# Kernel tuning notes

Measured on AMD Instinct MI355X. Metric: run time of the kernel, lower is better.

## Reference

```python
import jax, jax.numpy as jnp
import numpy as np

N = 100000   # nodes per graph (50k users + 50k items)
E = 1600000  # edges per graph
D = 128      # feature / hidden dim
B = 100000   # train pairs per domain
NUM_USER = 50000
LAMBDA = 1.0


def setup_inputs() -> dict:
    key = jax.random.key(0)
    ks = jax.random.split(key, 24)
    s = 1.0 / np.sqrt(D)
    return {
        "feats_s": jax.random.normal(ks[0], (N, D), jnp.float32),
        "feats_t": jax.random.normal(ks[1], (N, D), jnp.float32),
        "W1": jax.random.normal(ks[2], (D, D), jnp.float32) * s,
        "b1": jnp.zeros((D,), jnp.float32),
        "W2": jax.random.normal(ks[3], (D, D), jnp.float32) * s,
        "b2": jnp.zeros((D,), jnp.float32),
        "cls_W": jax.random.normal(ks[4], (2 * D, 1), jnp.float32) * s,
        "cls_b": jnp.zeros((1,), jnp.float32),
        "du_W": jax.random.normal(ks[5], (D, 1), jnp.float32) * s,
        "du_b": jnp.zeros((1,), jnp.float32),
        "di_W": jax.random.normal(ks[6], (D, 1), jnp.float32) * s,
        "di_b": jnp.zeros((1,), jnp.float32),
        "edge_src_s": jax.random.randint(ks[7], (E,), 0, N, jnp.int32),
        "edge_dst_s": jax.random.randint(ks[8], (E,), 0, N, jnp.int32),
        "edge_src_t": jax.random.randint(ks[9], (E,), 0, N, jnp.int32),
        "edge_dst_t": jax.random.randint(ks[10], (E,), 0, N, jnp.int32),
        "user_s": jax.random.randint(ks[11], (B,), 0, NUM_USER, jnp.int32),
        "item_s": jax.random.randint(ks[12], (B,), 0, NUM_USER, jnp.int32),
        "labels_s": jax.random.randint(ks[13], (B,), 0, 2, jnp.int32),
        "user_t": jax.random.randint(ks[14], (B,), 0, NUM_USER, jnp.int32),
        "item_t": jax.random.randint(ks[15], (B,), 0, NUM_USER, jnp.int32),
        "labels_t": jax.random.randint(ks[16], (B,), 0, 2, jnp.int32),
        "num_user_ds": NUM_USER,
        "num_user_dt": NUM_USER,
    }


def _gcn_layer(x, W, b, src, dst, dinv):
    # PyG GCNConv: out[i] = sum_{j->i} dinv[j]*dinv[i] * (x @ W)[j] + b
    h = x @ W
    norm = (dinv[src] * dinv[dst])[:, None]
    return jax.ops.segment_sum(h[src] * norm, dst, num_segments=x.shape[0]) + b


def _encode(x, src, dst, W1, b1, W2, b2):
    n = x.shape[0]
    sl = jnp.arange(n, dtype=src.dtype)            # self loops
    src = jnp.concatenate([src, sl])
    dst = jnp.concatenate([dst, sl])
    deg = jax.ops.segment_sum(jnp.ones_like(dst, dtype=x.dtype), dst, num_segments=n)
    dinv = jax.lax.rsqrt(jnp.maximum(deg, 1.0))    # deg >= 1 due to self loops
    h = jax.nn.relu(_gcn_layer(x, W1, b1, src, dst, dinv))
    return _gcn_layer(h, W2, b2, src, dst, dinv)   # dropout is identity at eval


def _bce_from_logits(z, y):
    # mean BCE on sigmoid(z), numerically stable
    return jnp.mean(y * jax.nn.softplus(-z) + (1.0 - y) * jax.nn.softplus(z))


def reference(feats_s, feats_t, W1, b1, W2, b2, cls_W, cls_b, du_W, du_b, di_W, di_b,
              edge_src_s, edge_dst_s, edge_src_t, edge_dst_t,
              user_s, item_s, labels_s, user_t, item_t, labels_t,
              num_user_ds, num_user_dt):
    x_ds = _encode(feats_s, edge_src_s, edge_dst_s, W1, b1, W2, b2)
    x_dt = _encode(feats_t, edge_src_t, edge_dst_t, W1, b1, W2, b2)

    ufs = x_ds[user_s]
    ifs = x_ds[item_s + num_user_ds]
    uft = x_dt[user_t]
    ift = x_dt[item_t + num_user_dt]

    z_s = (jnp.concatenate([ufs, ifs], axis=1) @ cls_W).reshape(-1) + cls_b[0]
    z_t = (jnp.concatenate([uft, ift], axis=1) @ cls_W).reshape(-1) + cls_b[0]
    clf_loss = _bce_from_logits(z_s, labels_s.astype(jnp.float32)) + \
               _bce_from_logits(z_t, labels_t.astype(jnp.float32))

    cu_s = jax.nn.sigmoid((ufs @ du_W).reshape(-1) + du_b[0])
    cu_t = jax.nn.sigmoid((uft @ du_W).reshape(-1) + du_b[0])
    ci_s = jax.nn.sigmoid((ifs @ di_W).reshape(-1) + di_b[0])
    ci_t = jax.nn.sigmoid((ift @ di_W).reshape(-1) + di_b[0])
    domain_loss = jnp.abs(jnp.mean(cu_s) - jnp.mean(cu_t)) + \
                  jnp.abs(jnp.mean(ci_s) - jnp.mean(ci_t))

    return clf_loss + LAMBDA * domain_loss
```

## Files before the change

kernel.cpp:

```cpp
#include <hip/hip_runtime.h>

#define D 128
#define NB 512
#define BSLACK 4112
#define CHUNK 8

typedef __attribute__((ext_vector_type(8))) short bf16x8;
typedef __attribute__((ext_vector_type(4))) float f32x4;
typedef __attribute__((ext_vector_type(2))) float f32x2;
typedef __attribute__((ext_vector_type(4))) int i32x4;

static __device__ inline unsigned pack_bf16x2(float a, float b) {
    unsigned ua = __float_as_uint(a);
    unsigned ub = __float_as_uint(b);
    ua += 0x7fffu + ((ua >> 16) & 1u);
    ub += 0x7fffu + ((ub >> 16) & 1u);
    return (ua >> 16) | (ub & 0xffff0000u);
}

__global__ __launch_bounds__(256) void bh_k(const int* __restrict__ dst_s,
                                            const int* __restrict__ dst_t,
                                            int* __restrict__ bcnt, int E) {
    int d = blockIdx.y;
    const int* dst = d ? dst_t : dst_s;
    __shared__ int h[NB];
    for (int i = threadIdx.x; i < NB; i += 256) h[i] = 0;
    __syncthreads();
    int stride = gridDim.x * 256;
    for (int e = blockIdx.x * 256 + threadIdx.x; e < E; e += stride)
        atomicAdd(&h[dst[e] >> 8], 1);
    __syncthreads();
    for (int i = threadIdx.x; i < NB; i += 256)
        if (h[i]) atomicAdd(&bcnt[d * NB + i], h[i]);
}

__global__ __launch_bounds__(1024) void scanB_k(const int* __restrict__ bcnt,
                                                int* __restrict__ bbase,
                                                int* __restrict__ cursor) {
    __shared__ int sh[1024];
    int t = threadIdx.x;
    int v = bcnt[t];
    sh[t] = v;
    __syncthreads();
    for (int o = 1; o < 1024; o <<= 1) {
        int x = (t >= o) ? sh[t - o] : 0;
        __syncthreads();
        sh[t] += x;
        __syncthreads();
    }
    int ex = sh[t] - v;
    bbase[t] = ex; cursor[t] = ex;
    if (t == 1023) bbase[1024] = sh[1023];
}

__global__ __launch_bounds__(256) void bin_k(const int* __restrict__ src_s,
                                             const int* __restrict__ dst_s,
                                             const int* __restrict__ src_t,
                                             const int* __restrict__ dst_t,
                                             int* __restrict__ cursor,
                                             unsigned* __restrict__ pairs, int E) {
    int d = blockIdx.y;
    const int* src = d ? src_t : src_s;
    const int* dst = d ? dst_t : dst_s;
    int* cur = cursor + d * NB;
    __shared__ int h[NB];
    __shared__ int gb[NB];
    int t0 = blockIdx.x * 2048;
    if (t0 >= E) return;
    for (int i = threadIdx.x; i < NB; i += 256) h[i] = 0;
    __syncthreads();
    int rank[8]; unsigned pk[8]; short bk[8];
    #pragma unroll
    for (int j = 0; j < 8; ++j) {
        int e = t0 + j * 256 + threadIdx.x;
        if (e < E) {
            int dd = dst[e], s = src[e];
            bk[j] = (short)(dd >> 8);
            pk[j] = (unsigned)s | ((unsigned)(dd & 255) << 24);
            rank[j] = atomicAdd(&h[dd >> 8], 1);
        } else bk[j] = -1;
    }
    __syncthreads();
    for (int i = threadIdx.x; i < NB; i += 256)
        gb[i] = h[i] ? atomicAdd(&cur[i], h[i]) : 0;
    __syncthreads();
    #pragma unroll
    for (int j = 0; j < 8; ++j)
        if (bk[j] >= 0) pairs[gb[bk[j]] + rank[j]] = pk[j];
}

__global__ __launch_bounds__(256) void csrb_k(const unsigned* __restrict__ pairs,
                                              const int* __restrict__ bbase,
                                              int2* __restrict__ nspan,
                                              float* __restrict__ dinv,
                                              int* __restrict__ csr, int N) {
    int d = blockIdx.y, bx = blockIdx.x, t = threadIdx.x;
    int g = d * NB + bx;
    int e0 = bbase[g], e1 = bbase[g + 1];
    int cbase = ((e0 + 15) & ~15) + g * BSLACK;
    float* dv = dinv + (size_t)d * (N + 1);
    int2* ns = nspan + (size_t)d * N;
    __shared__ int lh[256];
    __shared__ int lex[256];
    __shared__ int lc[256];
    lh[t] = 0; lc[t] = 0;
    __syncthreads();
    for (int e = e0 + t; e < e1; e += 256)
        atomicAdd(&lh[pairs[e] >> 24], 1);
    __syncthreads();
    int node = (bx << 8) + t;
    bool valid = node < N;
    int deg = lh[t];
    int pdeg = valid ? (((deg + 16) >> 4) << 4) : 0;
    lex[t] = pdeg;
    __syncthreads();
    for (int o = 1; o < 256; o <<= 1) {
        int x = (t >= o) ? lex[t - o] : 0;
        __syncthreads();
        lex[t] += x;
        __syncthreads();
    }
    int start = cbase + lex[t] - pdeg;
    if (valid) {
        ns[node] = make_int2(start, start + pdeg);
        dv[node] = rsqrtf((float)(deg + 1));
    }
    lex[t] = start;
    __syncthreads();
    for (int e = e0 + t; e < e1; e += 256) {
        unsigned p = pairs[e];
        int dn = p >> 24;
        int rank = atomicAdd(&lc[dn], 1);
        csr[lex[dn] + rank] = (int)(p & 0xffffffu);
    }
    __syncthreads();
    if (valid) {
        int b = lex[t];
        csr[b + deg] = node;
        for (int k = deg + 1; k < pdeg; ++k) csr[b + k] = N;
    }
    if (bx == 0 && t == 0) dv[N] = 0.f;
}

__global__ __launch_bounds__(256) void packW_k(const float* __restrict__ W1,
                                               const float* __restrict__ W2,
                                               unsigned short* __restrict__ wp1,
                                               unsigned short* __restrict__ wp2) {
    const float* W = blockIdx.x ? W2 : W1;
    unsigned short* wp = blockIdx.x ? wp2 : wp1;
    for (int idx = threadIdx.x; idx < 2048; idx += 256) {
        int f = idx >> 6, lane = idx & 63;
        int t = f >> 2, c = f & 3;
        int q = lane >> 4, nn = lane & 15;
        #pragma unroll
        for (int j = 0; j < 8; ++j) {
            unsigned u = __float_as_uint(W[(c * 32 + q * 8 + j) * 128 + t * 16 + nn]);
            u += 0x7fffu + ((u >> 16) & 1u);
            wp[idx * 8 + j] = (unsigned short)(u >> 16);
        }
    }
}

__global__ __launch_bounds__(256) void gemm_mfma(const void* __restrict__ xs,
                                                 const void* __restrict__ xt,
                                                 const unsigned short* __restrict__ wp,
                                                 unsigned* __restrict__ hb,
                                                 const float* __restrict__ dinv,
                                                 int N, int in_bf16) {
    int d = blockIdx.y;
    const void* xin = d ? xt : xs;
    unsigned* out = hb + (size_t)d * (N + 1) * 32;
    const float* dv = dinv + (size_t)d * (N + 1);
    __shared__ float cs[64 * 132];
    int tid = threadIdx.x;
    int wave = tid >> 6, lane = tid & 63;
    int quad = lane >> 4, nn = lane & 15;
    long long blockbase = (long long)blockIdx.x * 64;
    long long ar = blockbase + wave * 16 + nn;
    if (ar > N - 1) ar = N - 1;

    bf16x8 a[4];
    if (in_bf16) {
        const uint4* xr = (const uint4*)((const unsigned short*)xin + ar * 128);
        #pragma unroll
        for (int c = 0; c < 4; ++c) {
            union { uint4 u; bf16x8 v; } cv;
            cv.u = xr[c * 4 + quad];
            a[c] = cv.v;
        }
    } else {
        const float4* xr = (const float4*)((const float*)xin + ar * 128);
        #pragma unroll
        for (int c = 0; c < 4; ++c) {
            float4 lo = xr[c * 8 + quad * 2];
            float4 hi = xr[c * 8 + quad * 2 + 1];
            union { bf16x8 v; unsigned u[4]; } au;
            au.u[0] = pack_bf16x2(lo.x, lo.y);
            au.u[1] = pack_bf16x2(lo.z, lo.w);
            au.u[2] = pack_bf16x2(hi.x, hi.y);
            au.u[3] = pack_bf16x2(hi.z, hi.w);
            a[c] = au.v;
        }
    }

    f32x4 acc[8];
    #pragma unroll
    for (int t = 0; t < 8; ++t) acc[t] = (f32x4){0.f, 0.f, 0.f, 0.f};
    const bf16x8* wf = (const bf16x8*)wp;
    #pragma unroll
    for (int t = 0; t < 8; ++t) {
        #pragma unroll
        for (int c = 0; c < 4; ++c) {
            bf16x8 b = wf[(t * 4 + c) * 64 + lane];
            acc[t] = __builtin_amdgcn_mfma_f32_16x16x32_bf16(a[c], b, acc[t], 0, 0, 0);
        }
    }

    #pragma unroll
    for (int t = 0; t < 8; ++t) {
        #pragma unroll
        for (int r = 0; r < 4; ++r)
            cs[(wave * 16 + quad * 4 + r) * 132 + t * 16 + nn] = acc[t][r];
    }
    __syncthreads();

    #pragma unroll
    for (int i = 0; i < 8; ++i) {
        int idx = tid + i * 256;
        int r = idx >> 5, c4 = idx & 31;
        long long row = blockbase + r;
        if (row <= N) {
            float s = dv[row];
            const float4 v = *(const float4*)&cs[r * 132 + c4 * 4];
            int pk = __builtin_amdgcn_cvt_pk_fp8_f32(v.x * s, v.y * s, 0, false);
            pk = __builtin_amdgcn_cvt_pk_fp8_f32(v.z * s, v.w * s, pk, true);
            out[row * 32 + c4] = (unsigned)pk;
        }
    }
}

#define AGG_WINDOW(hsl, p0, p1)                                                 \
        unsigned u0 = hsl[(unsigned)p0.x << 5];                                 \
        unsigned u1 = hsl[(unsigned)p0.y << 5];                                 \
        unsigned u2 = hsl[(unsigned)p0.z << 5];                                 \
        unsigned u3 = hsl[(unsigned)p0.w << 5];                                 \
        unsigned u4 = hsl[(unsigned)p1.x << 5];                                 \
        unsigned u5 = hsl[(unsigned)p1.y << 5];                                 \
        unsigned u6 = hsl[(unsigned)p1.z << 5];                                 \
        unsigned u7 = hsl[(unsigned)p1.w << 5];                                 \
        f32x2 lo, hi;                                                           \
        lo = __builtin_amdgcn_cvt_pk_f32_fp8((int)u0, false);                   \
        hi = __builtin_amdgcn_cvt_pk_f32_fp8((int)u0, true);                    \
        s01 += lo; s23 += hi;                                                   \
        lo = __builtin_amdgcn_cvt_pk_f32_fp8((int)u1, false);                   \
        hi = __builtin_amdgcn_cvt_pk_f32_fp8((int)u1, true);                    \
        s01 += lo; s23 += hi;                                                   \
        lo = __builtin_amdgcn_cvt_pk_f32_fp8((int)u2, false);                   \
        hi = __builtin_amdgcn_cvt_pk_f32_fp8((int)u2, true);                    \
        s01 += lo; s23 += hi;                                                   \
        lo = __builtin_amdgcn_cvt_pk_f32_fp8((int)u3, false);                   \
        hi = __builtin_amdgcn_cvt_pk_f32_fp8((int)u3, true);                    \
        s01 += lo; s23 += hi;                                                   \
        lo = __builtin_amdgcn_cvt_pk_f32_fp8((int)u4, false);                   \
        hi = __builtin_amdgcn_cvt_pk_f32_fp8((int)u4, true);                    \
        s01 += lo; s23 += hi;                                                   \
        lo = __builtin_amdgcn_cvt_pk_f32_fp8((int)u5, false);                   \
        hi = __builtin_amdgcn_cvt_pk_f32_fp8((int)u5, true);                    \
        s01 += lo; s23 += hi;                                                   \
        lo = __builtin_amdgcn_cvt_pk_f32_fp8((int)u6, false);                   \
        hi = __builtin_amdgcn_cvt_pk_f32_fp8((int)u6, true);                    \
        s01 += lo; s23 += hi;                                                   \
        lo = __builtin_amdgcn_cvt_pk_f32_fp8((int)u7, false);                   \
        hi = __builtin_amdgcn_cvt_pk_f32_fp8((int)u7, true);                    \
        s01 += lo; s23 += hi;

__global__ __launch_bounds__(256) void agg1_k(const unsigned* __restrict__ hb,
                                              const float* __restrict__ dinv,
                                              const int2* __restrict__ nspan,
                                              const int* __restrict__ csr,
                                              const float* __restrict__ bias,
                                              uint2* __restrict__ abuf, int N) {
    int d = blockIdx.y;
    const unsigned* hs = hb + (size_t)d * (N + 1) * 32;
    const float* dv = dinv + (size_t)d * (N + 1);
    const int2* ns = nspan + (size_t)d * N;
    uint2* out = abuf + (size_t)d * N * 32;
    int wave = threadIdx.x >> 6, lane = threadIdx.x & 63;
    int node0 = (blockIdx.x * 4 + wave) * CHUNK;
    if (node0 >= N) return;
    int cnt = min(CHUNK, N - node0);
    int half = lane >> 5, li = lane & 31;
    int lc = lane & (CHUNK - 1);
    int2 myns = make_int2(0, 0);
    float mydv = 0.f;
    if (lc < cnt) { myns = ns[node0 + lc]; mydv = dv[node0 + lc]; }
    float4 b4 = ((const float4*)bias)[li];
    const unsigned* hsl = hs + li;
    const int* cp = csr + 8 * half;

    int k = 0;
    int e = __shfl(myns.x, 0);
    int end = __shfl(myns.y, 0);
    f32x2 s01 = (f32x2){0.f, 0.f};
    f32x2 s23 = (f32x2){0.f, 0.f};
    i32x4 c0 = __builtin_nontemporal_load((const i32x4*)(cp + e));
    i32x4 c1 = __builtin_nontemporal_load((const i32x4*)(cp + e + 4));
    for (;;) {
        i32x4 p0 = c0, p1 = c1;
        int en = e + 16;
        c0 = __builtin_nontemporal_load((const i32x4*)(cp + en));
        c1 = __builtin_nontemporal_load((const i32x4*)(cp + en + 4));
        AGG_WINDOW(hsl, p0, p1)
        if (en >= end) {
            float a0 = s01[0], a1 = s01[1], a2 = s23[0], a3 = s23[1];
            a0 += __shfl_xor(a0, 32);
            a1 += __shfl_xor(a1, 32);
            a2 += __shfl_xor(a2, 32);
            a3 += __shfl_xor(a3, 32);
            float dik = __shfl(mydv, k);
            float o0 = fmaxf(fmaf(dik, a0, b4.x), 0.f);
            float o1 = fmaxf(fmaf(dik, a1, b4.y), 0.f);
            float o2 = fmaxf(fmaf(dik, a2, b4.z), 0.f);
            float o3 = fmaxf(fmaf(dik, a3, b4.w), 0.f);
            if (half == 0)
                out[(size_t)(node0 + k) * 32 + li] =
                    make_uint2(pack_bf16x2(o0, o1), pack_bf16x2(o2, o3));
            if (++k >= cnt) break;
            end = __shfl(myns.y, k);
            s01 = (f32x2){0.f, 0.f};
            s23 = (f32x2){0.f, 0.f};
        }
        e = en;
    }
}

__global__ __launch_bounds__(256) void agg2_k(const unsigned* __restrict__ hb,
                                              const float* __restrict__ dinv,
                                              const int2* __restrict__ nspan,
                                              const int* __restrict__ csr,
                                              const float* __restrict__ bias,
                                              const float* __restrict__ clsW,
                                              const float* __restrict__ duW,
                                              const float* __restrict__ diW,
                                              const int* __restrict__ nus,
                                              const int* __restrict__ nut,
                                              float2* __restrict__ nodeDots, int N) {
    int d = blockIdx.y;
    const unsigned* hs = hb + (size_t)d * (N + 1) * 32;
    const float* dv = dinv + (size_t)d * (N + 1);
    const int2* ns = nspan + (size_t)d * N;
    float2* nd = nodeDots + (size_t)d * N;
    int nu = d ? nut[0] : nus[0];
    int wave = threadIdx.x >> 6, lane = threadIdx.x & 63;
    int node0 = (blockIdx.x * 4 + wave) * CHUNK;
    if (node0 >= N) return;
    int cnt = min(CHUNK, N - node0);
    int half = lane >> 5, li = lane & 31;
    int lc = lane & (CHUNK - 1);
    int2 myns = make_int2(0, 0);
    float mydv = 0.f;
    if (lc < cnt) { myns = ns[node0 + lc]; mydv = dv[node0 + lc]; }
    float4 b4 = ((const float4*)bias)[li];
    float4 wA0 = ((const float4*)clsW)[li];
    float4 wA1 = ((const float4*)clsW)[32 + li];
    float4 wB0 = ((const float4*)duW)[li];
    float4 wB1 = ((const float4*)diW)[li];
    const unsigned* hsl = hs + li;
    const int* cp = csr + 8 * half;

    int k = 0;
    int e = __shfl(myns.x, 0);
    int end = __shfl(myns.y, 0);
    f32x2 s01 = (f32x2){0.f, 0.f};
    f32x2 s23 = (f32x2){0.f, 0.f};
    i32x4 c0 = __builtin_nontemporal_load((const i32x4*)(cp + e));
    i32x4 c1 = __builtin_nontemporal_load((const i32x4*)(cp + e + 4));
    for (;;) {
        i32x4 p0 = c0, p1 = c1;
        int en = e + 16;
        c0 = __builtin_nontemporal_load((const i32x4*)(cp + en));
        c1 = __builtin_nontemporal_load((const i32x4*)(cp + en + 4));
        AGG_WINDOW(hsl, p0, p1)
        if (en >= end) {
            float a0 = s01[0], a1 = s01[1], a2 = s23[0], a3 = s23[1];
            a0 += __shfl_xor(a0, 32);
            a1 += __shfl_xor(a1, 32);
            a2 += __shfl_xor(a2, 32);
            a3 += __shfl_xor(a3, 32);
            float dik = __shfl(mydv, k);
            float o0 = fmaf(dik, a0, b4.x);
            float o1 = fmaf(dik, a1, b4.y);
            float o2 = fmaf(dik, a2, b4.z);
            float o3 = fmaf(dik, a3, b4.w);
            int nodek = node0 + k;
            int sel = (nodek >= nu) ? 1 : 0;
            float4 wA = sel ? wA1 : wA0;
            float4 wB = sel ? wB1 : wB0;
            float p = o0 * wA.x + o1 * wA.y + o2 * wA.z + o3 * wA.w;
            float q = o0 * wB.x + o1 * wB.y + o2 * wB.z + o3 * wB.w;
            #pragma unroll
            for (int o = 16; o > 0; o >>= 1) {
                p += __shfl_xor(p, o);
                q += __shfl_xor(q, o);
            }
            if (lane == 0) nd[nodek] = make_float2(p, q);
            if (++k >= cnt) break;
            end = __shfl(myns.y, k);
            s01 = (f32x2){0.f, 0.f};
            s23 = (f32x2){0.f, 0.f};
        }
        e = en;
    }
}

__global__ __launch_bounds__(256) void loss_k(const float2* __restrict__ nodeDots,
                                              const int* __restrict__ us, const int* __restrict__ is_,
                                              const int* __restrict__ ls,
                                              const int* __restrict__ ut, const int* __restrict__ it,
                                              const int* __restrict__ lt,
                                              const float* __restrict__ clsb,
                                              const float* __restrict__ dub,
                                              const float* __restrict__ dib,
                                              const int* __restrict__ nus,
                                              const int* __restrict__ nut,
                                              float* __restrict__ accum, int Bn, int N) {
    int d = blockIdx.y;
    const float2* nd = nodeDots + (size_t)d * N;
    const int* users = d ? ut : us;
    const int* items = d ? it : is_;
    const int* labels = d ? lt : ls;
    int nu = d ? nut[0] : nus[0];
    float* acc = accum + 3 * d;
    int k = blockIdx.x * 256 + threadIdx.x;
    float bce = 0.f, cu = 0.f, ci = 0.f;
    if (k < Bn) {
        int u = users[k];
        int t = items[k] + nu;
        float2 ud = nd[u];
        float2 id = nd[t];
        float z = ud.x + id.x + clsb[0];
        float y = (float)labels[k];
        float sp = fmaxf(z, 0.f) + log1pf(expf(-fabsf(z)));
        bce = sp - y * z;
        cu = 1.f / (1.f + expf(-(ud.y + dub[0])));
        ci = 1.f / (1.f + expf(-(id.y + dib[0])));
    }
    #pragma unroll
    for (int o = 32; o > 0; o >>= 1) {
        bce += __shfl_xor(bce, o);
        cu += __shfl_xor(cu, o);
        ci += __shfl_xor(ci, o);
    }
    __shared__ float sh[12];
    int lane = threadIdx.x & 63, wave = threadIdx.x >> 6;
    if (lane == 0) { sh[wave * 3 + 0] = bce; sh[wave * 3 + 1] = cu; sh[wave * 3 + 2] = ci; }
    __syncthreads();
    if (threadIdx.x < 3) {
        float v = sh[threadIdx.x] + sh[3 + threadIdx.x] + sh[6 + threadIdx.x] + sh[9 + threadIdx.x];
        atomicAdd(&acc[threadIdx.x], v);
    }
}

__global__ void finalize_k(const float* __restrict__ accum, float* __restrict__ out, float invB) {
    if (threadIdx.x == 0 && blockIdx.x == 0) {
        float clf = (accum[0] + accum[3]) * invB;
        float dom = fabsf((accum[1] - accum[4]) * invB) + fabsf((accum[2] - accum[5]) * invB);
        out[0] = clf + dom;
    }
}

extern "C" void kernel_launch(void* const* d_in, const int* in_sizes, int n_in,
                              void* d_out, int out_size, void* d_ws, size_t ws_size,
                              hipStream_t stream) {
    const float* feats_s = (const float*)d_in[0];
    const float* feats_t = (const float*)d_in[1];
    const float* W1   = (const float*)d_in[2];
    const float* b1   = (const float*)d_in[3];
    const float* W2   = (const float*)d_in[4];
    const float* b2   = (const float*)d_in[5];
    const float* clsW = (const float*)d_in[6];
    const float* clsb = (const float*)d_in[7];
    const float* duW  = (const float*)d_in[8];
    const float* dub  = (const float*)d_in[9];
    const float* diW  = (const float*)d_in[10];
    const float* dib  = (const float*)d_in[11];

    int N = in_sizes[0] / D;
    int E = in_sizes[12];
    int B = in_sizes[16];
    int nb = (N + 255) >> 8;

    char* ws = (char*)d_ws;
    size_t off = 0;
    auto alloc = [&](size_t bytes) -> void* {
        void* p = ws + off;
        off += (bytes + 255) & ~(size_t)255;
        return p;
    };
    int*      bcnt   = (int*)  alloc(2 * NB * 4);
    int*      bbase  = (int*)  alloc((2 * NB + 1) * 4);
    int*      cursor = (int*)  alloc(2 * NB * 4);
    float*    dinv   = (float*)alloc((size_t)2 * (N + 1) * 4);
    int2*     nspan  = (int2*) alloc((size_t)2 * N * 8);
    unsigned* pairs  = (unsigned*)alloc((size_t)2 * E * 4);
    int*      csr    = (int*)  alloc(((size_t)2 * E + 2 * NB * BSLACK + 256) * 4);
    unsigned* hbuf8  = (unsigned*)alloc((size_t)2 * (N + 1) * 128);
    unsigned* abuf   = (unsigned*)alloc((size_t)2 * N * 256);
    float2*   nodeDots = (float2*)alloc((size_t)2 * N * 8);
    unsigned short* wp1 = (unsigned short*)alloc(16384 * 2);
    unsigned short* wp2 = (unsigned short*)alloc(16384 * 2);
    float*    accum  = (float*)alloc(128);

    hipMemsetAsync(accum, 0, 6 * sizeof(float), stream);
    hipMemsetAsync(bcnt, 0, 2 * NB * 4, stream);

    const int* esrc_s = (const int*)d_in[12];
    const int* edst_s = (const int*)d_in[13];
    const int* esrc_t = (const int*)d_in[14];
    const int* edst_t = (const int*)d_in[15];
    const int* user_s = (const int*)d_in[16];
    const int* item_s = (const int*)d_in[17];
    const int* lab_s  = (const int*)d_in[18];
    const int* user_t = (const int*)d_in[19];
    const int* item_t = (const int*)d_in[20];
    const int* lab_t  = (const int*)d_in[21];
    const int* nup_s  = (const int*)d_in[22];
    const int* nup_t  = (const int*)d_in[23];

    packW_k<<<2, 256, 0, stream>>>(W1, W2, wp1, wp2);

    bh_k<<<dim3(512, 2), 256, 0, stream>>>(edst_s, edst_t, bcnt, E);
    scanB_k<<<1, 1024, 0, stream>>>(bcnt, bbase, cursor);
    bin_k<<<dim3((E + 2047) / 2048, 2), 256, 0, stream>>>(esrc_s, edst_s, esrc_t, edst_t,
                                                          cursor, pairs, E);
    csrb_k<<<dim3(nb, 2), 256, 0, stream>>>(pairs, bbase, nspan, dinv, csr, N);

    int ngb = (N + 64) / 64;
    int nchunk = (N + CHUNK - 1) / CHUNK;
    gemm_mfma<<<dim3(ngb, 2), 256, 0, stream>>>(feats_s, feats_t, wp1, hbuf8, dinv, N, 0);
    agg1_k<<<dim3((nchunk + 3) / 4, 2), 256, 0, stream>>>(hbuf8, dinv, nspan, csr, b1,
                                                          (uint2*)abuf, N);
    gemm_mfma<<<dim3(ngb, 2), 256, 0, stream>>>(abuf, abuf + (size_t)N * 64, wp2,
                                                hbuf8, dinv, N, 1);
    agg2_k<<<dim3((nchunk + 3) / 4, 2), 256, 0, stream>>>(hbuf8, dinv, nspan, csr, b2,
                                                          clsW, duW, diW, nup_s, nup_t,
                                                          nodeDots, N);
    loss_k<<<dim3((B + 255) / 256, 2), 256, 0, stream>>>(nodeDots,
                                                         user_s, item_s, lab_s,
                                                         user_t, item_t, lab_t,
                                                         clsb, dub, dib, nup_s, nup_t,
                                                         accum, B, N);
    finalize_k<<<1, 64, 0, stream>>>(accum, (float*)d_out, 1.0f / (float)B);
}
```

Measured before the change: 486.7 us.

## Software-pipeline edge gathers in aggregation kernels with 8-byte loads and XCD-aware block mapping

The aggregation kernels are restructured so each lane gathers 8 bytes (8 fp8 features) per neighbor, with four row groups of 16 lanes instead of two halves of 32. A three-stage rotating pipeline keeps index loads and feature gathers for upcoming windows in flight while the current one is accumulated, hiding gather latency. Blocks are remapped so each graph domain lands on a fixed subset of XCDs to improve L2 locality, and the CSR padding slack is enlarged so the deeper lookahead reads stay in bounds. The cost is more registers, an extra cross-lane reduction step, and more wasted padding reads at span ends.

Result: slower. 522.2 us (+7.3%).

```diff
diff --git a/kernel.cpp b/kernel.cpp
--- a/kernel.cpp
+++ b/kernel.cpp
@@ -2,7 +2,7 @@
 
 #define D 128
 #define NB 512
-#define BSLACK 4112
+#define BSLACK 4160
 #define CHUNK 8
 
 typedef __attribute__((ext_vector_type(8))) short bf16x8;
@@ -138,6 +138,10 @@
         int b = lex[t];
         csr[b + deg] = node;
         for (int k = deg + 1; k < pdeg; ++k) csr[b + k] = N;
+    }
+    if (t == 255) {
+        int bend = start + pdeg;
+        for (int i = 0; i < 48; ++i) csr[bend + i] = N;
     }
     if (bx == 0 && t == 0) dv[N] = 0.f;
 }
@@ -239,178 +243,193 @@
     }
 }
 
-#define AGG_WINDOW(hsl, p0, p1)                                                 \
-        unsigned u0 = hsl[(unsigned)p0.x << 5];                                 \
-        unsigned u1 = hsl[(unsigned)p0.y << 5];                                 \
-        unsigned u2 = hsl[(unsigned)p0.z << 5];                                 \
-        unsigned u3 = hsl[(unsigned)p0.w << 5];                                 \
-        unsigned u4 = hsl[(unsigned)p1.x << 5];                                 \
-        unsigned u5 = hsl[(unsigned)p1.y << 5];                                 \
-        unsigned u6 = hsl[(unsigned)p1.z << 5];                                 \
-        unsigned u7 = hsl[(unsigned)p1.w << 5];                                 \
-        f32x2 lo, hi;                                                           \
-        lo = __builtin_amdgcn_cvt_pk_f32_fp8((int)u0, false);                   \
-        hi = __builtin_amdgcn_cvt_pk_f32_fp8((int)u0, true);                    \
-        s01 += lo; s23 += hi;                                                   \
-        lo = __builtin_amdgcn_cvt_pk_f32_fp8((int)u1, false);                   \
-        hi = __builtin_amdgcn_cvt_pk_f32_fp8((int)u1, true);                    \
-        s01 += lo; s23 += hi;                                                   \
-        lo = __builtin_amdgcn_cvt_pk_f32_fp8((int)u2, false);                   \
-        hi = __builtin_amdgcn_cvt_pk_f32_fp8((int)u2, true);                    \
-        s01 += lo; s23 += hi;                                                   \
-        lo = __builtin_amdgcn_cvt_pk_f32_fp8((int)u3, false);                   \
-        hi = __builtin_amdgcn_cvt_pk_f32_fp8((int)u3, true);                    \
-        s01 += lo; s23 += hi;                                                   \
-        lo = __builtin_amdgcn_cvt_pk_f32_fp8((int)u4, false);                   \
-        hi = __builtin_amdgcn_cvt_pk_f32_fp8((int)u4, true);                    \
-        s01 += lo; s23 += hi;                                                   \
-        lo = __builtin_amdgcn_cvt_pk_f32_fp8((int)u5, false);                   \
-        hi = __builtin_amdgcn_cvt_pk_f32_fp8((int)u5, true);                    \
-        s01 += lo; s23 += hi;                                                   \
-        lo = __builtin_amdgcn_cvt_pk_f32_fp8((int)u6, false);                   \
-        hi = __builtin_amdgcn_cvt_pk_f32_fp8((int)u6, true);                    \
-        s01 += lo; s23 += hi;                                                   \
-        lo = __builtin_amdgcn_cvt_pk_f32_fp8((int)u7, false);                   \
-        hi = __builtin_amdgcn_cvt_pk_f32_fp8((int)u7, true);                    \
-        s01 += lo; s23 += hi;
+#define NTLD(p) __builtin_nontemporal_load((const i32x4*)(p))
+
+#define GATHER(g0, g1, g2, g3, c)                                            \
+        g0 = *(const uint2*)(hsl + (((unsigned)(c).x) << 5));                \
+        g1 = *(const uint2*)(hsl + (((unsigned)(c).y) << 5));                \
+        g2 = *(const uint2*)(hsl + (((unsigned)(c).z) << 5));                \
+        g3 = *(const uint2*)(hsl + (((unsigned)(c).w) << 5));
+
+#define CONS1(g)                                                             \
+        { f32x2 lo, hi;                                                      \
+          lo = __builtin_amdgcn_cvt_pk_f32_fp8((int)(g).x, false);           \
+          hi = __builtin_amdgcn_cvt_pk_f32_fp8((int)(g).x, true);            \
+          s0 += lo; s1 += hi;                                                \
+          lo = __builtin_amdgcn_cvt_pk_f32_fp8((int)(g).y, false);           \
+          hi = __builtin_amdgcn_cvt_pk_f32_fp8((int)(g).y, true);            \
+          s2 += lo; s3 += hi; }
+
+#define BOUND                                                                \
+        if (en >= end) {                                                     \
+            finalize(k);                                                     \
+            if (++k >= cnt) break;                                           \
+            end = __shfl(myns.y, k);                                         \
+            s0 = s1 = s2 = s3 = (f32x2){0.f, 0.f};                           \
+        }                                                                    \
+        e = en;
+
+#define AGG_PIPE_LOOP                                                        \
+    i32x4 ca = NTLD(cp + e), cb = NTLD(cp + e + 16), cc = NTLD(cp + e + 32); \
+    uint2 A0, A1, A2, A3, B0, B1, B2, B3, C0, C1, C2, C3;                    \
+    GATHER(A0, A1, A2, A3, ca)                                               \
+    GATHER(B0, B1, B2, B3, cb)                                               \
+    for (;;) {                                                               \
+        int en;                                                              \
+        ca = NTLD(cp + e + 48);                                              \
+        GATHER(C0, C1, C2, C3, cc)                                           \
+        CONS1(A0) CONS1(A1) CONS1(A2) CONS1(A3)                              \
+        en = e + 16; BOUND                                                   \
+        cb = NTLD(cp + e + 48);                                              \
+        GATHER(A0, A1, A2, A3, ca)                                           \
+        CONS1(B0) CONS1(B1) CONS1(B2) CONS1(B3)                              \
+        en = e + 16; BOUND                                                   \
+        cc = NTLD(cp + e + 48);                                              \
+        GATHER(B0, B1, B2, B3, cb)                                           \
+        CONS1(C0) CONS1(C1) CONS1(C2) CONS1(C3)                              \
+        en = e + 16; BOUND                                                   \
+    }
 
 __global__ __launch_bounds__(256) void agg1_k(const unsigned* __restrict__ hb,
                                               const float* __restrict__ dinv,
                                               const int2* __restrict__ nspan,
                                               const int* __restrict__ csr,
-                                              const float* __restrict__ bias,
-                                              uint2* __restrict__ abuf, int N) {
-    int d = blockIdx.y;
+                                              const float* __restrict__ b1,
+                                              const float* __restrict__ b1t,
+                                              uint4* __restrict__ abuf,
+                                              int N, int nblk) {
+    int lin = blockIdx.x;
+    int xcd = lin & 7;
+    int d = xcd >> 2;
+    int blkd = ((lin >> 3) << 2) + (xcd & 3);
+    int wave = threadIdx.x >> 6, lane = threadIdx.x & 63;
+    int node0 = (blkd * 4 + wave) * CHUNK;
+    if (node0 >= N) return;
     const unsigned* hs = hb + (size_t)d * (N + 1) * 32;
     const float* dv = dinv + (size_t)d * (N + 1);
     const int2* ns = nspan + (size_t)d * N;
-    uint2* out = abuf + (size_t)d * N * 32;
-    int wave = threadIdx.x >> 6, lane = threadIdx.x & 63;
-    int node0 = (blockIdx.x * 4 + wave) * CHUNK;
-    if (node0 >= N) return;
+    uint4* out = abuf + (size_t)d * N * 16;
+    const float* bias = d ? b1t : b1;
     int cnt = min(CHUNK, N - node0);
-    int half = lane >> 5, li = lane & 31;
+    int rg = lane >> 4, fo = lane & 15;
     int lc = lane & (CHUNK - 1);
     int2 myns = make_int2(0, 0);
     float mydv = 0.f;
     if (lc < cnt) { myns = ns[node0 + lc]; mydv = dv[node0 + lc]; }
-    float4 b4 = ((const float4*)bias)[li];
-    const unsigned* hsl = hs + li;
-    const int* cp = csr + 8 * half;
+    float4 bA = ((const float4*)bias)[2 * fo];
+    float4 bB = ((const float4*)bias)[2 * fo + 1];
+    const unsigned* hsl = hs + (fo << 1);
+    const int* cp = csr + (rg << 2);
+
+    f32x2 s0 = (f32x2){0.f, 0.f}, s1 = s0, s2 = s0, s3 = s0;
+
+    auto finalize = [&](int kk) {
+        float a[8] = {s0[0], s0[1], s1[0], s1[1], s2[0], s2[1], s3[0], s3[1]};
+        #pragma unroll
+        for (int i = 0; i < 8; ++i) {
+            a[i] += __shfl_xor(a[i], 16);
+            a[i] += __shfl_xor(a[i], 32);
+        }
+        float dik = __shfl(mydv, kk);
+        float o0 = fmaxf(fmaf(dik, a[0], bA.x), 0.f);
+        float o1 = fmaxf(fmaf(dik, a[1], bA.y), 0.f);
+        float o2 = fmaxf(fmaf(dik, a[2], bA.z), 0.f);
+        float o3 = fmaxf(fmaf(dik, a[3], bA.w), 0.f);
+        float o4 = fmaxf(fmaf(dik, a[4], bB.x), 0.f);
+        float o5 = fmaxf(fmaf(dik, a[5], bB.y), 0.f);
+        float o6 = fmaxf(fmaf(dik, a[6], bB.z), 0.f);
+        float o7 = fmaxf(fmaf(dik, a[7], bB.w), 0.f);
+        if (lane < 16)
+            out[(size_t)(node0 + kk) * 16 + fo] =
+                make_uint4(pack_bf16x2(o0, o1), pack_bf16x2(o2, o3),
+                           pack_bf16x2(o4, o5), pack_bf16x2(o6, o7));
+    };
 
     int k = 0;
     int e = __shfl(myns.x, 0);
     int end = __shfl(myns.y, 0);
-    f32x2 s01 = (f32x2){0.f, 0.f};
-    f32x2 s23 = (f32x2){0.f, 0.f};
-    i32x4 c0 = __builtin_nontemporal_load((const i32x4*)(cp + e));
-    i32x4 c1 = __builtin_nontemporal_load((const i32x4*)(cp + e + 4));
-    for (;;) {
-        i32x4 p0 = c0, p1 = c1;
-        int en = e + 16;
-        c0 = __builtin_nontemporal_load((const i32x4*)(cp + en));
-        c1 = __builtin_nontemporal_load((const i32x4*)(cp + en + 4));
-        AGG_WINDOW(hsl, p0, p1)
-        if (en >= end) {
-            float a0 = s01[0], a1 = s01[1], a2 = s23[0], a3 = s23[1];
-            a0 += __shfl_xor(a0, 32);
-            a1 += __shfl_xor(a1, 32);
-            a2 += __shfl_xor(a2, 32);
-            a3 += __shfl_xor(a3, 32);
-            float dik = __shfl(mydv, k);
-            float o0 = fmaxf(fmaf(dik, a0, b4.x), 0.f);
-            float o1 = fmaxf(fmaf(dik, a1, b4.y), 0.f);
-            float o2 = fmaxf(fmaf(dik, a2, b4.z), 0.f);
-            float o3 = fmaxf(fmaf(dik, a3, b4.w), 0.f);
-            if (half == 0)
-                out[(size_t)(node0 + k) * 32 + li] =
-                    make_uint2(pack_bf16x2(o0, o1), pack_bf16x2(o2, o3));
-            if (++k >= cnt) break;
-            end = __shfl(myns.y, k);
-            s01 = (f32x2){0.f, 0.f};
-            s23 = (f32x2){0.f, 0.f};
-        }
-        e = en;
-    }
+    AGG_PIPE_LOOP
 }
 
 __global__ __launch_bounds__(256) void agg2_k(const unsigned* __restrict__ hb,
                                               const float* __restrict__ dinv,
                                               const int2* __restrict__ nspan,
                                               const int* __restrict__ csr,
-                                              const float* __restrict__ bias,
+                                              const float* __restrict__ b2,
+                                              const float* __restrict__ b2t,
                                               const float* __restrict__ clsW,
                                               const float* __restrict__ duW,
                                               const float* __restrict__ diW,
                                               const int* __restrict__ nus,
                                               const int* __restrict__ nut,
-                                              float2* __restrict__ nodeDots, int N) {
-    int d = blockIdx.y;
+                                              float2* __restrict__ nodeDots,
+                                              int N, int nblk) {
+    int lin = blockIdx.x;
+    int xcd = lin & 7;
+    int d = xcd >> 2;
+    int blkd = ((lin >> 3) << 2) + (xcd & 3);
+    int wave = threadIdx.x >> 6, lane = threadIdx.x & 63;
+    int node0 = (blkd * 4 + wave) * CHUNK;
+    if (node0 >= N) return;
     const unsigned* hs = hb + (size_t)d * (N + 1) * 32;
     const float* dv = dinv + (size_t)d * (N + 1);
     const int2* ns = nspan + (size_t)d * N;
     float2* nd = nodeDots + (size_t)d * N;
+    const float* bias = d ? b2t : b2;
     int nu = d ? nut[0] : nus[0];
-    int wave = threadIdx.x >> 6, lane = threadIdx.x & 63;
-    int node0 = (blockIdx.x * 4 + wave) * CHUNK;
-    if (node0 >= N) return;
     int cnt = min(CHUNK, N - node0);
-    int half = lane >> 5, li = lane & 31;
+    int rg = lane >> 4, fo = lane & 15;
     int lc = lane & (CHUNK - 1);
     int2 myns = make_int2(0, 0);
     float mydv = 0.f;
     if (lc < cnt) { myns = ns[node0 + lc]; mydv = dv[node0 + lc]; }
-    float4 b4 = ((const float4*)bias)[li];
-    float4 wA0 = ((const float4*)clsW)[li];
-    float4 wA1 = ((const float4*)clsW)[32 + li];
-    float4 wB0 = ((const float4*)duW)[li];
-    float4 wB1 = ((const float4*)diW)[li];
-    const unsigned* hsl = hs + li;
-    const int* cp = csr + 8 * half;
+    float4 bA = ((const float4*)bias)[2 * fo];
+    float4 bB = ((const float4*)bias)[2 * fo + 1];
+    const unsigned* hsl = hs + (fo << 1);
+    const int* cp = csr + (rg << 2);
+
+    f32x2 s0 = (f32x2){0.f, 0.f}, s1 = s0, s2 = s0, s3 = s0;
+
+    auto finalize = [&](int kk) {
+        float a[8] = {s0[0], s0[1], s1[0], s1[1], s2[0], s2[1], s3[0], s3[1]};
+        #pragma unroll
+        for (int i = 0; i < 8; ++i) {
+            a[i] += __shfl_xor(a[i], 16);
+            a[i] += __shfl_xor(a[i], 32);
+        }
+        float dik = __shfl(mydv, kk);
+        float o0 = fmaf(dik, a[0], bA.x);
+        float o1 = fmaf(dik, a[1], bA.y);
+        float o2 = fmaf(dik, a[2], bA.z);
+        float o3 = fmaf(dik, a[3], bA.w);
+        float o4 = fmaf(dik, a[4], bB.x);
+        float o5 = fmaf(dik, a[5], bB.y);
+        float o6 = fmaf(dik, a[6], bB.z);
+        float o7 = fmaf(dik, a[7], bB.w);
+        int nodek = node0 + kk;
+        int sel = (nodek >= nu) ? 1 : 0;
+        const float4* cw = (const float4*)clsW;
+        float4 wa0 = cw[sel * 32 + 2 * fo];
+        float4 wa1 = cw[sel * 32 + 2 * fo + 1];
+        const float4* bw = (const float4*)(sel ? diW : duW);
+        float4 wb0 = bw[2 * fo];
+        float4 wb1 = bw[2 * fo + 1];
+        float p = o0 * wa0.x + o1 * wa0.y + o2 * wa0.z + o3 * wa0.w +
+                  o4 * wa1.x + o5 * wa1.y + o6 * wa1.z + o7 * wa1.w;
+        float q = o0 * wb0.x + o1 * wb0.y + o2 * wb0.z + o3 * wb0.w +
+                  o4 * wb1.x + o5 * wb1.y + o6 * wb1.z + o7 * wb1.w;
+        #pragma unroll
+        for (int o = 8; o > 0; o >>= 1) {
+            p += __shfl_xor(p, o);
+            q += __shfl_xor(q, o);
+        }
+        if (lane == 0) nd[nodek] = make_float2(p, q);
+    };
 
     int k = 0;
     int e = __shfl(myns.x, 0);
     int end = __shfl(myns.y, 0);
-    f32x2 s01 = (f32x2){0.f, 0.f};
-    f32x2 s23 = (f32x2){0.f, 0.f};
-    i32x4 c0 = __builtin_nontemporal_load((const i32x4*)(cp + e));
-    i32x4 c1 = __builtin_nontemporal_load((const i32x4*)(cp + e + 4));
-    for (;;) {
-        i32x4 p0 = c0, p1 = c1;
-        int en = e + 16;
-        c0 = __builtin_nontemporal_load((const i32x4*)(cp + en));
-        c1 = __builtin_nontemporal_load((const i32x4*)(cp + en + 4));
-        AGG_WINDOW(hsl, p0, p1)
-        if (en >= end) {
-            float a0 = s01[0], a1 = s01[1], a2 = s23[0], a3 = s23[1];
-            a0 += __shfl_xor(a0, 32);
-            a1 += __shfl_xor(a1, 32);
-            a2 += __shfl_xor(a2, 32);
-            a3 += __shfl_xor(a3, 32);
-            float dik = __shfl(mydv, k);
-            float o0 = fmaf(dik, a0, b4.x);
-            float o1 = fmaf(dik, a1, b4.y);
-            float o2 = fmaf(dik, a2, b4.z);
-            float o3 = fmaf(dik, a3, b4.w);
-            int nodek = node0 + k;
-            int sel = (nodek >= nu) ? 1 : 0;
-            float4 wA = sel ? wA1 : wA0;
-            float4 wB = sel ? wB1 : wB0;
-            float p = o0 * wA.x + o1 * wA.y + o2 * wA.z + o3 * wA.w;
-            float q = o0 * wB.x + o1 * wB.y + o2 * wB.z + o3 * wB.w;
-            #pragma unroll
-            for (int o = 16; o > 0; o >>= 1) {
-                p += __shfl_xor(p, o);
-                q += __shfl_xor(q, o);
-            }
-            if (lane == 0) nd[nodek] = make_float2(p, q);
-            if (++k >= cnt) break;
-            end = __shfl(myns.y, k);
-            s01 = (f32x2){0.f, 0.f};
-            s23 = (f32x2){0.f, 0.f};
-        }
-        e = en;
-    }
+    AGG_PIPE_LOOP
 }
 
 __global__ __launch_bounds__(256) void loss_k(const float2* __restrict__ nodeDots,
@@ -537,14 +556,16 @@
 
     int ngb = (N + 64) / 64;
     int nchunk = (N + CHUNK - 1) / CHUNK;
+    int nblk = (nchunk + 3) / 4;
+    int gx = 8 * ((nblk + 3) / 4);
     gemm_mfma<<<dim3(ngb, 2), 256, 0, stream>>>(feats_s, feats_t, wp1, hbuf8, dinv, N, 0);
-    agg1_k<<<dim3((nchunk + 3) / 4, 2), 256, 0, stream>>>(hbuf8, dinv, nspan, csr, b1,
-                                                          (uint2*)abuf, N);
+    agg1_k<<<gx, 256, 0, stream>>>(hbuf8, dinv, nspan, csr, b1, b1,
+                                   (uint4*)abuf, N, nblk);
     gemm_mfma<<<dim3(ngb, 2), 256, 0, stream>>>(abuf, abuf + (size_t)N * 64, wp2,
                                                 hbuf8, dinv, N, 1);
-    agg2_k<<<dim3((nchunk + 3) / 4, 2), 256, 0, stream>>>(hbuf8, dinv, nspan, csr, b2,
-                                                          clsW, duW, diW, nup_s, nup_t,
-                                                          nodeDots, N);
+    agg2_k<<<gx, 256, 0, stream>>>(hbuf8, dinv, nspan, csr, b2, b2,
+                                   clsW, duW, diW, nup_s, nup_t,
+                                   nodeDots, N, nblk);
     loss_k<<<dim3((B + 255) / 256, 2), 256, 0, stream>>>(nodeDots,
                                                          user_s, item_s, lab_s,
                                                          user_t, item_t, lab_t,
```
